# Performance work log

Hardware: AMD Instinct MI355X
Metric: run time of the kernel (lower is better)

Reference implementation:

```python
import jax, jax.numpy as jnp
import numpy as np

B, C, N, D = 8, 64, 512, 64

def setup_inputs() -> dict:
    key = jax.random.key(0)
    k1, = jax.random.split(key, 1)
    inp = jax.random.normal(k1, (B, C, N, D), dtype=jnp.float32)
    a = jnp.full((1, C, 1, 1), 0.75, dtype=jnp.float32)
    b = jnp.full((1, C, 1, 1), 0.25, dtype=jnp.float32)
    return {"inp": inp, "a": a, "b": b}

def reference(inp, a, b):
    # A = inp @ inp^T : [B, C, N, N]
    A = jnp.einsum('bcnd,bcmd->bcnm', inp, inp)
    # B = A @ A : [B, C, N, N]
    B2 = jnp.einsum('bcnk,bckm->bcnm', A, A)
    Mat = -a * A + b * B2
    # out = inp + Mat @ inp : [B, C, N, D]
    out = inp + jnp.einsum('bcnm,bcmd->bcnd', Mat, inp)
    return out
```

## Files before the change

kernel.cpp:

```cpp
#include <hip/hip_runtime.h>


typedef __bf16 bf16;
typedef __attribute__((ext_vector_type(8)))  __bf16 bf16x8;
typedef __attribute__((ext_vector_type(4)))  __bf16 bf16x4;
typedef __attribute__((ext_vector_type(16))) float  f32x16;

namespace {

__device__ __forceinline__ int sxz(int d) { return ((d >> 1) ^ (d >> 4)) & 7; }

__global__ __launch_bounds__(512, 4)
void ns_mfma(const float* __restrict__ inp, const float* __restrict__ aw,
             const float* __restrict__ bw, float* __restrict__ out) {
    __shared__ unsigned char smem[54272] __attribute__((aligned(128)));
    bf16*  const Xt0 = (bf16*)smem;
    bf16*  const Xt1 = (bf16*)(smem + 9216);
    bf16*  const Xr  = (bf16*)smem;
    float* const Gp  = (float*)(smem + 18432);
    bf16*  const Gbf = (bf16*)(smem + 35840);
    bf16*  const Hbf = (bf16*)(smem + 45056);

    const int slice = blockIdx.x;
    const float* __restrict__ X = inp + (size_t)slice * (512 * 64);
    float* __restrict__ O       = out + (size_t)slice * (512 * 64);

    const int t    = threadIdx.x;
    const int lane = t & 63;
    const int w    = t >> 6;
    const int l31  = lane & 31;
    const int l5   = lane >> 5;
    const int half = t >> 8;
    const int th   = t & 255;
    const int s_nq = th >> 4;
    const int s_dq = th & 15;

    const float* __restrict__ Xbase =
        X + (size_t)(64 * half + 4 * s_nq) * 64 + 4 * s_dq;

    float4 rv[2][4];
#pragma unroll
    for (int rn = 0; rn < 4; ++rn)
        rv[0][rn] = *(const float4*)&Xbase[(size_t)rn * 64];

    const float av = aw[slice & 63];
    const float bv = bw[slice & 63];

    f32x16 acc;
#pragma unroll
    for (int q = 0; q < 16; ++q) acc[q] = 0.f;

    bf16* const XtMine = half ? Xt1 : Xt0;
    const int tile = w & 3;
    const int i32  = (tile >> 1) * 32;
    const int j32  = (tile & 1) * 32;
    const int rowA = i32 + l31;
    const int rowB = j32 + l31;
    const int sA   = sxz(rowA);
    const int sB   = sxz(rowB);

    bf16x4 xr[4][4];

#pragma unroll
    for (int it = 0; it < 4; ++it) {
        if (it < 3) {
#pragma unroll
            for (int rn = 0; rn < 4; ++rn)
                rv[(it + 1) & 1][rn] =
                    *(const float4*)&Xbase[(size_t)(128 * (it + 1) + rn) * 64];
        }
#pragma unroll
        for (int rn = 0; rn < 4; ++rn) {
            const float4 v = rv[it & 1][rn];
            xr[it][rn][0] = (bf16)v.x; xr[it][rn][1] = (bf16)v.y;
            xr[it][rn][2] = (bf16)v.z; xr[it][rn][3] = (bf16)v.w;
        }
#pragma unroll
        for (int r = 0; r < 4; ++r) {
            const int d = 4 * s_dq + r;
            bf16x4 v;
            v[0] = xr[it][0][r]; v[1] = xr[it][1][r];
            v[2] = xr[it][2][r]; v[3] = xr[it][3][r];
            const int g = ((s_nq >> 1) ^ sxz(d)) & 7;
            *(bf16x4*)&XtMine[d * 72 + g * 8 + 4 * (s_nq & 1)] = v;
        }
        __syncthreads();
#pragma unroll
        for (int ks = 0; ks < 4; ++ks) {
            const int gw = 2 * ks + l5;
            bf16x8 a = *(const bf16x8*)&XtMine[rowA * 72 + ((gw ^ sA) & 7) * 8];
            bf16x8 b = *(const bf16x8*)&XtMine[rowB * 72 + ((gw ^ sB) & 7) * 8];
            acc = __builtin_amdgcn_mfma_f32_32x32x16_bf16(a, b, acc, 0, 0, 0);
        }
        __syncthreads();
    }

    if (half == 0) {
#pragma unroll
        for (int q = 0; q < 16; ++q) {
            const int r = (q & 3) + 8 * (q >> 2) + 4 * l5;
            Gp[(i32 + r) * 68 + j32 + l31] = acc[q];
        }
    }
#pragma unroll
    for (int rn = 0; rn < 4; ++rn)
        *(bf16x4*)&Xr[(64 * half + 4 * s_nq + rn) * 72 + 4 * s_dq] = xr[0][rn];
    __syncthreads();
    if (half == 1) {
#pragma unroll
        for (int q = 0; q < 16; ++q) {
            const int r  = (q & 3) + 8 * (q >> 2) + 4 * l5;
            const int ii = i32 + r;
            const int jj = j32 + l31;
            Gbf[ii * 72 + jj] = (bf16)(acc[q] + Gp[ii * 68 + jj]);
        }
    }
    __syncthreads();

    if (w < 4) {
        const int pi = (w >> 1) * 32;
        const int pj = (w & 1) * 32;
        f32x16 h;
#pragma unroll
        for (int q = 0; q < 16; ++q) h[q] = 0.f;
#pragma unroll
        for (int ks = 0; ks < 4; ++ks) {
            bf16x8 a = *(const bf16x8*)&Gbf[(pi + l31) * 72 + ks * 16 + 8 * l5];
            bf16x8 b = *(const bf16x8*)&Gbf[(pj + l31) * 72 + ks * 16 + 8 * l5];
            h = __builtin_amdgcn_mfma_f32_32x32x16_bf16(a, b, h, 0, 0, 0);
        }
#pragma unroll
        for (int q = 0; q < 16; ++q) {
            const int r  = (q & 3) + 8 * (q >> 2) + 4 * l5;
            const int ii = pi + r;
            const int jj = pj + l31;
            Hbf[ii * 72 + jj] = (bf16)(bv * h[q] - av * (float)Gbf[ii * 72 + jj]);
        }
    }
    __syncthreads();

    const int nb = (w >> 1) * 32;
    const int db = (w & 1) * 32;

#pragma unroll
    for (int it = 0; it < 4; ++it) {
        f32x16 o;
#pragma unroll
        for (int q = 0; q < 16; ++q) o[q] = 0.f;
#pragma unroll
        for (int ks = 0; ks < 4; ++ks) {
            bf16x8 a = *(const bf16x8*)&Xr [(nb + l31) * 72 + ks * 16 + 8 * l5];
            bf16x8 b = *(const bf16x8*)&Hbf[(db + l31) * 72 + ks * 16 + 8 * l5];
            o = __builtin_amdgcn_mfma_f32_32x32x16_bf16(a, b, o, 0, 0, 0);
        }
#pragma unroll
        for (int q = 0; q < 16; ++q) {
            const int rl = (q & 3) + 8 * (q >> 2) + 4 * l5;
            const int nl = nb + rl;
            const int d  = db + l31;
            O[(size_t)(it * 128 + nl) * 64 + d] = o[q] + (float)Xr[nl * 72 + d];
        }
        if (it < 3) {
            __syncthreads();
#pragma unroll
            for (int rn = 0; rn < 4; ++rn)
                *(bf16x4*)&Xr[(64 * half + 4 * s_nq + rn) * 72 + 4 * s_dq] = xr[it + 1][rn];
            __syncthreads();
        }
    }
}

}

extern "C" void kernel_launch(void* const* d_in, const int* in_sizes, int n_in,
                              void* d_out, int out_size, void* d_ws, size_t ws_size,
                              hipStream_t stream) {
    const float* inp = (const float*)d_in[0];
    const float* aw  = (const float*)d_in[1];
    const float* bw  = (const float*)d_in[2];
    float* out       = (float*)d_out;

    ns_mfma<<<dim3(512), dim3(512), 0, stream>>>(inp, aw, bw, out);
}
```

Baseline: 26.57 us.

## Process two slices per block, prefetching the second slice during the first

Each block now handles two (b,c) slices sequentially and launches 256 blocks instead of 512. The second slice's whole input is loaded into registers during the first slice's Gram pass, so its global load latency is hidden behind the first slice's compute and stores. Shared memory grows to about 71 KB and launch bounds drop to 2 blocks per CU. The cost is much higher register pressure (64 extra floats held per thread), lower occupancy, and only 256 blocks, which may underfill the GPU's CUs.

```diff
diff --git a/kernel.cpp b/kernel.cpp
--- a/kernel.cpp
+++ b/kernel.cpp
@@ -10,20 +10,133 @@
 
 __device__ __forceinline__ int sxz(int d) { return ((d >> 1) ^ (d >> 4)) & 7; }
 
-__global__ __launch_bounds__(512, 4)
-void ns_mfma(const float* __restrict__ inp, const float* __restrict__ aw,
+__device__ __forceinline__ bf16x4 cvt4(const float4 v) {
+    bf16x4 r;
+    r[0] = (bf16)v.x; r[1] = (bf16)v.y; r[2] = (bf16)v.z; r[3] = (bf16)v.w;
+    return r;
+}
+
+__device__ __forceinline__ void stage_chunk(bf16* XtMine, const bf16x4 (&x)[4],
+                                            int s_nq, int s_dq) {
+#pragma unroll
+    for (int r = 0; r < 4; ++r) {
+        const int d = 4 * s_dq + r;
+        bf16x4 v;
+        v[0] = x[0][r]; v[1] = x[1][r]; v[2] = x[2][r]; v[3] = x[3][r];
+        const int g = ((s_nq >> 1) ^ sxz(d)) & 7;
+        *(bf16x4*)&XtMine[d * 72 + g * 8 + 4 * (s_nq & 1)] = v;
+    }
+}
+
+__device__ __forceinline__ void mfma4(const bf16* XtMine, f32x16& acc,
+                                      int rowA, int rowB, int sA, int sB, int l5) {
+#pragma unroll
+    for (int ks = 0; ks < 4; ++ks) {
+        const int gw = 2 * ks + l5;
+        bf16x8 a = *(const bf16x8*)&XtMine[rowA * 72 + ((gw ^ sA) & 7) * 8];
+        bf16x8 b = *(const bf16x8*)&XtMine[rowB * 72 + ((gw ^ sB) & 7) * 8];
+        acc = __builtin_amdgcn_mfma_f32_32x32x16_bf16(a, b, acc, 0, 0, 0);
+    }
+}
+
+__device__ __forceinline__ void make_H(const f32x16& acc, float av, float bv,
+                                       bf16* Xr, const bf16x4 (&xr0)[4],
+                                       float* Gp, bf16* Gbf, bf16* Hbf,
+                                       int half, int w, int l31, int l5,
+                                       int i32, int j32, int s_nq, int s_dq) {
+    if (half == 0) {
+#pragma unroll
+        for (int q = 0; q < 16; ++q) {
+            const int r = (q & 3) + 8 * (q >> 2) + 4 * l5;
+            Gp[(i32 + r) * 68 + j32 + l31] = acc[q];
+        }
+    }
+#pragma unroll
+    for (int rn = 0; rn < 4; ++rn)
+        *(bf16x4*)&Xr[(64 * half + 4 * s_nq + rn) * 72 + 4 * s_dq] = xr0[rn];
+    __syncthreads();
+    if (half == 1) {
+#pragma unroll
+        for (int q = 0; q < 16; ++q) {
+            const int r  = (q & 3) + 8 * (q >> 2) + 4 * l5;
+            const int ii = i32 + r;
+            const int jj = j32 + l31;
+            Gbf[ii * 72 + jj] = (bf16)(acc[q] + Gp[ii * 68 + jj]);
+        }
+    }
+    __syncthreads();
+    if (w < 4) {
+        const int pi = (w >> 1) * 32;
+        const int pj = (w & 1) * 32;
+        f32x16 h;
+#pragma unroll
+        for (int q = 0; q < 16; ++q) h[q] = 0.f;
+#pragma unroll
+        for (int ks = 0; ks < 4; ++ks) {
+            bf16x8 a = *(const bf16x8*)&Gbf[(pi + l31) * 72 + ks * 16 + 8 * l5];
+            bf16x8 b = *(const bf16x8*)&Gbf[(pj + l31) * 72 + ks * 16 + 8 * l5];
+            h = __builtin_amdgcn_mfma_f32_32x32x16_bf16(a, b, h, 0, 0, 0);
+        }
+#pragma unroll
+        for (int q = 0; q < 16; ++q) {
+            const int r  = (q & 3) + 8 * (q >> 2) + 4 * l5;
+            const int ii = pi + r;
+            const int jj = pj + l31;
+            Hbf[ii * 72 + jj] = (bf16)(bv * h[q] - av * (float)Gbf[ii * 72 + jj]);
+        }
+    }
+    __syncthreads();
+}
+
+__device__ __forceinline__ void pass3(bf16* Xr, const bf16x4 (&xr)[4][4],
+                                      const bf16* Hbf, float* O,
+                                      int half, int l31, int l5, int nb, int db,
+                                      int s_nq, int s_dq) {
+#pragma unroll
+    for (int it = 0; it < 4; ++it) {
+        f32x16 o;
+#pragma unroll
+        for (int q = 0; q < 16; ++q) o[q] = 0.f;
+#pragma unroll
+        for (int ks = 0; ks < 4; ++ks) {
+            bf16x8 a = *(const bf16x8*)&Xr [(nb + l31) * 72 + ks * 16 + 8 * l5];
+            bf16x8 b = *(const bf16x8*)&Hbf[(db + l31) * 72 + ks * 16 + 8 * l5];
+            o = __builtin_amdgcn_mfma_f32_32x32x16_bf16(a, b, o, 0, 0, 0);
+        }
+#pragma unroll
+        for (int q = 0; q < 16; ++q) {
+            const int rl = (q & 3) + 8 * (q >> 2) + 4 * l5;
+            const int nl = nb + rl;
+            const int d  = db + l31;
+            O[(size_t)(it * 128 + nl) * 64 + d] = o[q] + (float)Xr[nl * 72 + d];
+        }
+        if (it < 3) {
+            __syncthreads();
+#pragma unroll
+            for (int rn = 0; rn < 4; ++rn)
+                *(bf16x4*)&Xr[(64 * half + 4 * s_nq + rn) * 72 + 4 * s_dq] = xr[it + 1][rn];
+            __syncthreads();
+        }
+    }
+}
+
+__global__ __launch_bounds__(512, 2)
+void ns_pair(const float* __restrict__ inp, const float* __restrict__ aw,
              const float* __restrict__ bw, float* __restrict__ out) {
-    __shared__ unsigned char smem[54272] __attribute__((aligned(128)));
-    bf16*  const Xt0 = (bf16*)smem;
-    bf16*  const Xt1 = (bf16*)(smem + 9216);
-    bf16*  const Xr  = (bf16*)smem;
-    float* const Gp  = (float*)(smem + 18432);
-    bf16*  const Gbf = (bf16*)(smem + 35840);
-    bf16*  const Hbf = (bf16*)(smem + 45056);
-
-    const int slice = blockIdx.x;
-    const float* __restrict__ X = inp + (size_t)slice * (512 * 64);
-    float* __restrict__ O       = out + (size_t)slice * (512 * 64);
+    __shared__ unsigned char smem[72704] __attribute__((aligned(128)));
+    bf16*  const SA  = (bf16*)smem;
+    bf16*  const SB  = (bf16*)(smem + 18432);
+    float* const Gp  = (float*)(smem + 36864);
+    bf16*  const Gbf = (bf16*)(smem + 54272);
+    bf16*  const Hbf = (bf16*)(smem + 63488);
+
+    const int blk    = blockIdx.x;
+    const int sliceA = 2 * blk;
+    const int sliceB = 2 * blk + 1;
+    const float* __restrict__ XA = inp + (size_t)sliceA * 32768;
+    const float* __restrict__ XB = inp + (size_t)sliceB * 32768;
+    float* __restrict__ OA       = out + (size_t)sliceA * 32768;
+    float* __restrict__ OB       = out + (size_t)sliceB * 32768;
 
     const int t    = threadIdx.x;
     const int lane = t & 63;
@@ -35,22 +148,17 @@
     const int s_nq = th >> 4;
     const int s_dq = th & 15;
 
-    const float* __restrict__ Xbase =
-        X + (size_t)(64 * half + 4 * s_nq) * 64 + 4 * s_dq;
+    const float* __restrict__ XbA = XA + (size_t)(64 * half + 4 * s_nq) * 64 + 4 * s_dq;
+    const float* __restrict__ XbB = XB + (size_t)(64 * half + 4 * s_nq) * 64 + 4 * s_dq;
 
     float4 rv[2][4];
 #pragma unroll
     for (int rn = 0; rn < 4; ++rn)
-        rv[0][rn] = *(const float4*)&Xbase[(size_t)rn * 64];
-
-    const float av = aw[slice & 63];
-    const float bv = bw[slice & 63];
-
-    f32x16 acc;
-#pragma unroll
-    for (int q = 0; q < 16; ++q) acc[q] = 0.f;
-
-    bf16* const XtMine = half ? Xt1 : Xt0;
+        rv[0][rn] = *(const float4*)&XbA[(size_t)rn * 64];
+
+    const float avA = aw[sliceA & 63], bvA = bw[sliceA & 63];
+    const float avB = aw[sliceB & 63], bvB = bw[sliceB & 63];
+
     const int tile = w & 3;
     const int i32  = (tile >> 1) * 32;
     const int j32  = (tile & 1) * 32;
@@ -58,8 +166,18 @@
     const int rowB = j32 + l31;
     const int sA   = sxz(rowA);
     const int sB   = sxz(rowB);
-
-    bf16x4 xr[4][4];
+    const int nb   = (w >> 1) * 32;
+    const int db   = (w & 1) * 32;
+
+    bf16* const XtA = SA + half * 4608;
+    bf16* const XtB = SB + half * 4608;
+
+    f32x16 acc;
+#pragma unroll
+    for (int q = 0; q < 16; ++q) acc[q] = 0.f;
+
+    bf16x4 xrA[4][4];
+    float4 rvB[4][4];
 
 #pragma unroll
     for (int it = 0; it < 4; ++it) {
@@ -67,107 +185,48 @@
 #pragma unroll
             for (int rn = 0; rn < 4; ++rn)
                 rv[(it + 1) & 1][rn] =
-                    *(const float4*)&Xbase[(size_t)(128 * (it + 1) + rn) * 64];
-        }
-#pragma unroll
-        for (int rn = 0; rn < 4; ++rn) {
-            const float4 v = rv[it & 1][rn];
-            xr[it][rn][0] = (bf16)v.x; xr[it][rn][1] = (bf16)v.y;
-            xr[it][rn][2] = (bf16)v.z; xr[it][rn][3] = (bf16)v.w;
-        }
-#pragma unroll
-        for (int r = 0; r < 4; ++r) {
-            const int d = 4 * s_dq + r;
-            bf16x4 v;
-            v[0] = xr[it][0][r]; v[1] = xr[it][1][r];
-            v[2] = xr[it][2][r]; v[3] = xr[it][3][r];
-            const int g = ((s_nq >> 1) ^ sxz(d)) & 7;
-            *(bf16x4*)&XtMine[d * 72 + g * 8 + 4 * (s_nq & 1)] = v;
-        }
-        __syncthreads();
-#pragma unroll
-        for (int ks = 0; ks < 4; ++ks) {
-            const int gw = 2 * ks + l5;
-            bf16x8 a = *(const bf16x8*)&XtMine[rowA * 72 + ((gw ^ sA) & 7) * 8];
-            bf16x8 b = *(const bf16x8*)&XtMine[rowB * 72 + ((gw ^ sB) & 7) * 8];
-            acc = __builtin_amdgcn_mfma_f32_32x32x16_bf16(a, b, acc, 0, 0, 0);
-        }
-        __syncthreads();
-    }
-
-    if (half == 0) {
-#pragma unroll
-        for (int q = 0; q < 16; ++q) {
-            const int r = (q & 3) + 8 * (q >> 2) + 4 * l5;
-            Gp[(i32 + r) * 68 + j32 + l31] = acc[q];
-        }
-    }
-#pragma unroll
-    for (int rn = 0; rn < 4; ++rn)
-        *(bf16x4*)&Xr[(64 * half + 4 * s_nq + rn) * 72 + 4 * s_dq] = xr[0][rn];
-    __syncthreads();
-    if (half == 1) {
-#pragma unroll
-        for (int q = 0; q < 16; ++q) {
-            const int r  = (q & 3) + 8 * (q >> 2) + 4 * l5;
-            const int ii = i32 + r;
-            const int jj = j32 + l31;
-            Gbf[ii * 72 + jj] = (bf16)(acc[q] + Gp[ii * 68 + jj]);
-        }
-    }
-    __syncthreads();
-
-    if (w < 4) {
-        const int pi = (w >> 1) * 32;
-        const int pj = (w & 1) * 32;
-        f32x16 h;
-#pragma unroll
-        for (int q = 0; q < 16; ++q) h[q] = 0.f;
-#pragma unroll
-        for (int ks = 0; ks < 4; ++ks) {
-            bf16x8 a = *(const bf16x8*)&Gbf[(pi + l31) * 72 + ks * 16 + 8 * l5];
-            bf16x8 b = *(const bf16x8*)&Gbf[(pj + l31) * 72 + ks * 16 + 8 * l5];
-            h = __builtin_amdgcn_mfma_f32_32x32x16_bf16(a, b, h, 0, 0, 0);
-        }
-#pragma unroll
-        for (int q = 0; q < 16; ++q) {
-            const int r  = (q & 3) + 8 * (q >> 2) + 4 * l5;
-            const int ii = pi + r;
-            const int jj = pj + l31;
-            Hbf[ii * 72 + jj] = (bf16)(bv * h[q] - av * (float)Gbf[ii * 72 + jj]);
-        }
-    }
-    __syncthreads();
-
-    const int nb = (w >> 1) * 32;
-    const int db = (w & 1) * 32;
+                    *(const float4*)&XbA[(size_t)(128 * (it + 1) + rn) * 64];
+        }
+        if (it == 2) {
+#pragma unroll
+            for (int s = 0; s < 4; ++s)
+#pragma unroll
+                for (int rn = 0; rn < 4; ++rn)
+                    rvB[s][rn] = *(const float4*)&XbB[(size_t)(128 * s + rn) * 64];
+        }
+#pragma unroll
+        for (int rn = 0; rn < 4; ++rn) xrA[it][rn] = cvt4(rv[it & 1][rn]);
+        stage_chunk(XtA, xrA[it], s_nq, s_dq);
+        __syncthreads();
+        mfma4(XtA, acc, rowA, rowB, sA, sB, l5);
+        __syncthreads();
+    }
+
+    make_H(acc, avA, bvA, SA, xrA[0], Gp, Gbf, Hbf,
+           half, w, l31, l5, i32, j32, s_nq, s_dq);
+    pass3(SA, xrA, Hbf, OA, half, l31, l5, nb, db, s_nq, s_dq);
+
+    bf16x4 xrB[4][4];
+#pragma unroll
+    for (int s = 0; s < 4; ++s)
+#pragma unroll
+        for (int rn = 0; rn < 4; ++rn) xrB[s][rn] = cvt4(rvB[s][rn]);
+
+    f32x16 accB;
+#pragma unroll
+    for (int q = 0; q < 16; ++q) accB[q] = 0.f;
 
 #pragma unroll
     for (int it = 0; it < 4; ++it) {
-        f32x16 o;
-#pragma unroll
-        for (int q = 0; q < 16; ++q) o[q] = 0.f;
-#pragma unroll
-        for (int ks = 0; ks < 4; ++ks) {
-            bf16x8 a = *(const bf16x8*)&Xr [(nb + l31) * 72 + ks * 16 + 8 * l5];
-            bf16x8 b = *(const bf16x8*)&Hbf[(db + l31) * 72 + ks * 16 + 8 * l5];
-            o = __builtin_amdgcn_mfma_f32_32x32x16_bf16(a, b, o, 0, 0, 0);
-        }
-#pragma unroll
-        for (int q = 0; q < 16; ++q) {
-            const int rl = (q & 3) + 8 * (q >> 2) + 4 * l5;
-            const int nl = nb + rl;
-            const int d  = db + l31;
-            O[(size_t)(it * 128 + nl) * 64 + d] = o[q] + (float)Xr[nl * 72 + d];
-        }
-        if (it < 3) {
-            __syncthreads();
-#pragma unroll
-            for (int rn = 0; rn < 4; ++rn)
-                *(bf16x4*)&Xr[(64 * half + 4 * s_nq + rn) * 72 + 4 * s_dq] = xr[it + 1][rn];
-            __syncthreads();
-        }
-    }
+        stage_chunk(XtB, xrB[it], s_nq, s_dq);
+        __syncthreads();
+        mfma4(XtB, accB, rowA, rowB, sA, sB, l5);
+        __syncthreads();
+    }
+
+    make_H(accB, avB, bvB, SB, xrB[0], Gp, Gbf, Hbf,
+           half, w, l31, l5, i32, j32, s_nq, s_dq);
+    pass3(SB, xrB, Hbf, OB, half, l31, l5, nb, db, s_nq, s_dq);
 }
 
 }
@@ -180,5 +239,5 @@
     const float* bw  = (const float*)d_in[2];
     float* out       = (float*)d_out;
 
-    ns_mfma<<<dim3(512), dim3(512), 0, stream>>>(inp, aw, bw, out);
-}
+    ns_pair<<<dim3(256), dim3(512), 0, stream>>>(inp, aw, bw, out);
+}
```

After: 28.17 us. 1.06x slower.
